# Kernel optimization log

Hardware: AMD Instinct MI355X
Metric: run time of the kernel (lower is better)

## Reference

```python
import jax, jax.numpy as jnp
import numpy as np

BETA = 0.25  # commitment_cost


def setup_inputs() -> dict:
    key = jax.random.key(0)
    k1, k2 = jax.random.split(key)
    B, T, K, D = 4096, 64, 512, 64
    z_e = jax.random.normal(k1, (B, T, D), dtype=jnp.float32)
    # torch init: uniform_(-1/K, 1/K) per slot codebook, stacked -> (T, K, D)
    codebooks = jax.random.uniform(k2, (T, K, D), dtype=jnp.float32,
                                   minval=-1.0 / K, maxval=1.0 / K)
    return {"z_e": z_e, "codebooks": codebooks}


def reference(z_e, codebooks):
    """ProductQuantizer.forward (use_ema=True, eval), vectorized over slots.

    z_e:       (B, T, D)
    codebooks: (T, K, D)
    Returns (z_q_st, tokens, vq_loss, utilization).
    """
    B, T, D = z_e.shape
    K = codebooks.shape[1]
    # squared-L2 distances per slot: (B, T, K)
    distances = (
        jnp.sum(z_e * z_e, axis=-1, keepdims=True)          # (B, T, 1)
        - 2.0 * jnp.einsum("btd,tkd->btk", z_e, codebooks)  # (B, T, K)
        + jnp.sum(codebooks * codebooks, axis=-1)[None]      # (1, T, K)
    )
    tokens = jnp.argmin(distances, axis=-1)                  # (B, T) int
    # gather nearest code per (batch, slot)
    z_q = codebooks[jnp.arange(T)[None, :], tokens]          # (B, T, D)
    # straight-through estimator
    z_q_st = z_e + jax.lax.stop_gradient(z_q - z_e)
    # use_ema=True branch: loss = mean_t( beta * mse(z_e_t, sg(z_q_t)) )
    # all slots have equal size, so this equals beta * global mean sq err
    vq_loss = BETA * jnp.mean(jnp.square(z_e - jax.lax.stop_gradient(z_q)))
    # utilization: fraction of (slot, code) pairs used at least once
    flat_idx = (jnp.arange(T)[None, :] * K + tokens).ravel()
    used = jnp.zeros((T * K,), dtype=z_e.dtype).at[flat_idx].set(1.0)
    utilization = jnp.sum(used) / (T * K)
    return z_q_st, tokens, vq_loss, utilization
```

## Files before the change

### kernel.cpp

```cpp
#include <hip/hip_runtime.h>

#define B_N 4096
#define T_N 64
#define K_N 512
#define D_N 64
#define KC 64
#define NCHUNK (K_N / KC)


__global__ __launch_bounds__(256) void prep_kernel(const float* __restrict__ cb,
                                                   float* __restrict__ c2,
                                                   unsigned* __restrict__ used,
                                                   double* __restrict__ loss) {
    int i = blockIdx.x * 256 + threadIdx.x;
    used[i] = 0u;
    if (i == 0) *loss = 0.0;
    const float4* c = reinterpret_cast<const float4*>(cb + (size_t)i * D_N);
    float s = 0.0f;
#pragma unroll
    for (int j = 0; j < 16; ++j) {
        float4 v = c[j];
        s = __fadd_rn(s, __fmul_rn(v.x, v.x));
        s = __fadd_rn(s, __fmul_rn(v.y, v.y));
        s = __fadd_rn(s, __fmul_rn(v.z, v.z));
        s = __fadd_rn(s, __fmul_rn(v.w, v.w));
    }
    c2[i] = s;
}

__global__ __launch_bounds__(256, 2) void vq_main(const float* __restrict__ z_e,
                                                  const float* __restrict__ cb,
                                                  const float* __restrict__ c2,
                                                  float* __restrict__ zq_out,
                                                  float* __restrict__ tok_out,
                                                  unsigned* __restrict__ used,
                                                  double* __restrict__ loss_sum) {
    const int t   = blockIdx.y;
    const int tid = threadIdx.x;
    const int b0  = blockIdx.x * 512 + 2 * tid;
    const int b1  = b0 + 1;

    __shared__ __align__(16) float cbuf[2][KC * D_N];
    __shared__ __align__(16) float c2buf[2][KC];

    float z0[D_N], z1[D_N];
    const float* zr0 = z_e + ((size_t)b0 * T_N + t) * D_N;
    const float* zr1 = z_e + ((size_t)b1 * T_N + t) * D_N;
#pragma unroll
    for (int j = 0; j < 16; ++j) {
        float4 v0 = reinterpret_cast<const float4*>(zr0)[j];
        float4 v1 = reinterpret_cast<const float4*>(zr1)[j];
        z0[4*j+0] = v0.x; z0[4*j+1] = v0.y; z0[4*j+2] = v0.z; z0[4*j+3] = v0.w;
        z1[4*j+0] = v1.x; z1[4*j+1] = v1.y; z1[4*j+2] = v1.z; z1[4*j+3] = v1.w;
    }

    float A0 = 0.0f, A1 = 0.0f;
#pragma unroll
    for (int d = 0; d < D_N; ++d) A0 = __fadd_rn(A0, __fmul_rn(z0[d], z0[d]));
#pragma unroll
    for (int d = 0; d < D_N; ++d) A1 = __fadd_rn(A1, __fmul_rn(z1[d], z1[d]));

    const float* cbt = cb + (size_t)t * K_N * D_N;
    const float* c2t = c2 + t * K_N;

    float4 pf[4];
    float4 c2pf;

    auto issue = [&](int c) {
        const float4* src = reinterpret_cast<const float4*>(cbt + (size_t)c * KC * D_N);
#pragma unroll
        for (int j = 0; j < 4; ++j) pf[j] = src[j * 256 + tid];
        if (tid < 16) c2pf = reinterpret_cast<const float4*>(c2t + c * KC)[tid];
    };
    auto writebuf = [&](int buf) {
#pragma unroll
        for (int j = 0; j < 4; ++j) reinterpret_cast<float4*>(cbuf[buf])[j * 256 + tid] = pf[j];
        if (tid < 16) reinterpret_cast<float4*>(c2buf[buf])[tid] = c2pf;
    };

    issue(0);
    writebuf(0);
    __syncthreads();

    float best0 = __builtin_inff(), best1 = __builtin_inff();
    int tok0 = 0, tok1 = 0;

    for (int c = 0; c < NCHUNK; ++c) {
        if (c < NCHUNK - 1) issue(c + 1);
        const float* cc  = cbuf[c & 1];
        const float* c2c = c2buf[c & 1];
        for (int kk = 0; kk < KC; ++kk) {
            const float* crow = cc + kk * D_N;
            float a0 = 0.0f, a1 = 0.0f;
#pragma unroll
            for (int d = 0; d < D_N; ++d) {
                float cd = crow[d];
                a0 = __builtin_fmaf(z0[d], cd, a0);
                a1 = __builtin_fmaf(z1[d], cd, a1);
            }
            float c2k = c2c[kk];
            float dist0 = __fadd_rn(__fsub_rn(A0, __fmul_rn(2.0f, a0)), c2k);
            float dist1 = __fadd_rn(__fsub_rn(A1, __fmul_rn(2.0f, a1)), c2k);
            int k = c * KC + kk;
            if (dist0 < best0) { best0 = dist0; tok0 = k; }
            if (dist1 < best1) { best1 = dist1; tok1 = k; }
        }
        if (c < NCHUNK - 1) {
            __syncthreads();
            writebuf((c + 1) & 1);
            __syncthreads();
        }
    }

    const float* q0 = cbt + (size_t)tok0 * D_N;
    const float* q1 = cbt + (size_t)tok1 * D_N;
    float* zq0 = zq_out + ((size_t)b0 * T_N + t) * D_N;
    float* zq1 = zq_out + ((size_t)b1 * T_N + t) * D_N;
    double ld = 0.0;
#pragma unroll
    for (int j = 0; j < 16; ++j) {
        float4 qv = reinterpret_cast<const float4*>(q0)[j];
        reinterpret_cast<float4*>(zq0)[j] = qv;
        float d0 = z0[4*j+0] - qv.x, d1 = z0[4*j+1] - qv.y;
        float d2 = z0[4*j+2] - qv.z, d3 = z0[4*j+3] - qv.w;
        ld += (double)d0*d0 + (double)d1*d1 + (double)d2*d2 + (double)d3*d3;
    }
#pragma unroll
    for (int j = 0; j < 16; ++j) {
        float4 qv = reinterpret_cast<const float4*>(q1)[j];
        reinterpret_cast<float4*>(zq1)[j] = qv;
        float d0 = z1[4*j+0] - qv.x, d1 = z1[4*j+1] - qv.y;
        float d2 = z1[4*j+2] - qv.z, d3 = z1[4*j+3] - qv.w;
        ld += (double)d0*d0 + (double)d1*d1 + (double)d2*d2 + (double)d3*d3;
    }
    tok_out[(size_t)b0 * T_N + t] = (float)tok0;
    tok_out[(size_t)b1 * T_N + t] = (float)tok1;
    used[t * K_N + tok0] = 1u;
    used[t * K_N + tok1] = 1u;

    __syncthreads();
    double* red = reinterpret_cast<double*>(cbuf[0]);
    red[tid] = ld;
    __syncthreads();
    for (int s = 128; s > 0; s >>= 1) {
        if (tid < s) red[tid] += red[tid + s];
        __syncthreads();
    }
    if (tid == 0) atomicAdd(loss_sum, red[0]);
}

__global__ __launch_bounds__(1024) void finalize_kernel(const unsigned* __restrict__ used,
                                                        const double* __restrict__ loss_sum,
                                                        float* __restrict__ out) {
    __shared__ unsigned s[1024];
    const uint4* u4 = reinterpret_cast<const uint4*>(used);
    unsigned c = 0;
#pragma unroll
    for (int i = 0; i < 8; ++i) {
        uint4 v = u4[threadIdx.x + i * 1024];
        c += v.x + v.y + v.z + v.w;
    }
    s[threadIdx.x] = c;
    __syncthreads();
    for (int st = 512; st > 0; st >>= 1) {
        if (threadIdx.x < st) s[threadIdx.x] += s[threadIdx.x + st];
        __syncthreads();
    }
    if (threadIdx.x == 0) {
        const size_t base = (size_t)B_N * T_N * D_N + (size_t)B_N * T_N;
        out[base]     = (float)(0.25 * (*loss_sum) / (double)((size_t)B_N * T_N * D_N));
        out[base + 1] = (float)s[0] / (float)(T_N * K_N);
    }
}

extern "C" void kernel_launch(void* const* d_in, const int* in_sizes, int n_in,
                              void* d_out, int out_size, void* d_ws, size_t ws_size,
                              hipStream_t stream) {
    const float* z_e = (const float*)d_in[0];
    const float* cb  = (const float*)d_in[1];
    float* out = (float*)d_out;

    float*    c2   = (float*)d_ws;
    unsigned* used = (unsigned*)((char*)d_ws + 131072);
    double*   loss = (double*)((char*)d_ws + 262144);

    prep_kernel<<<128, 256, 0, stream>>>(cb, c2, used, loss);

    float* tok_out = out + (size_t)B_N * T_N * D_N;
    vq_main<<<dim3(B_N / 512, T_N), 256, 0, stream>>>(z_e, cb, c2, out, tok_out, used, loss);

    finalize_kernel<<<1, 1024, 0, stream>>>(used, loss, out);
}
```

Before: 399.6 us.

## Read codebook rows directly from global memory and fold codebook norms into main kernel

Removes the double-buffered shared-memory staging of codebook chunks and has every thread read codebook rows straight from global memory. Each row address is uniform across the wavefront, so the loads can be served as scalar or broadcast loads through cache. Codebook squared norms are now computed per block into shared memory, which drops the separate prep kernel. The used/loss buffers are cleared with a memset instead. This trades the per-chunk block barriers for redundant norm computation in every block and a dependence on cache hits for the inner-loop loads.

```diff
diff --git a/kernel.cpp b/kernel.cpp
--- a/kernel.cpp
+++ b/kernel.cpp
@@ -4,33 +4,10 @@
 #define T_N 64
 #define K_N 512
 #define D_N 64
-#define KC 64
-#define NCHUNK (K_N / KC)
 
-
-__global__ __launch_bounds__(256) void prep_kernel(const float* __restrict__ cb,
-                                                   float* __restrict__ c2,
-                                                   unsigned* __restrict__ used,
-                                                   double* __restrict__ loss) {
-    int i = blockIdx.x * 256 + threadIdx.x;
-    used[i] = 0u;
-    if (i == 0) *loss = 0.0;
-    const float4* c = reinterpret_cast<const float4*>(cb + (size_t)i * D_N);
-    float s = 0.0f;
-#pragma unroll
-    for (int j = 0; j < 16; ++j) {
-        float4 v = c[j];
-        s = __fadd_rn(s, __fmul_rn(v.x, v.x));
-        s = __fadd_rn(s, __fmul_rn(v.y, v.y));
-        s = __fadd_rn(s, __fmul_rn(v.z, v.z));
-        s = __fadd_rn(s, __fmul_rn(v.w, v.w));
-    }
-    c2[i] = s;
-}
 
 __global__ __launch_bounds__(256, 2) void vq_main(const float* __restrict__ z_e,
                                                   const float* __restrict__ cb,
-                                                  const float* __restrict__ c2,
                                                   float* __restrict__ zq_out,
                                                   float* __restrict__ tok_out,
                                                   unsigned* __restrict__ used,
@@ -40,95 +17,92 @@
     const int b0  = blockIdx.x * 512 + 2 * tid;
     const int b1  = b0 + 1;
 
-    __shared__ __align__(16) float cbuf[2][KC * D_N];
-    __shared__ __align__(16) float c2buf[2][KC];
+    const float* cbt = cb + (size_t)t * K_N * D_N;
+
+    __shared__ float  c2s[K_N];
+    __shared__ double red[256];
+
+    {
+        const float4* c = reinterpret_cast<const float4*>(cbt) + (size_t)(2 * tid) * 16;
+        float s0 = 0.0f, s1 = 0.0f;
+#pragma unroll
+        for (int j = 0; j < 16; ++j) {
+            float4 v0 = c[j];
+            float4 v1 = c[16 + j];
+            s0 = __fadd_rn(s0, __fmul_rn(v0.x, v0.x));
+            s0 = __fadd_rn(s0, __fmul_rn(v0.y, v0.y));
+            s0 = __fadd_rn(s0, __fmul_rn(v0.z, v0.z));
+            s0 = __fadd_rn(s0, __fmul_rn(v0.w, v0.w));
+            s1 = __fadd_rn(s1, __fmul_rn(v1.x, v1.x));
+            s1 = __fadd_rn(s1, __fmul_rn(v1.y, v1.y));
+            s1 = __fadd_rn(s1, __fmul_rn(v1.z, v1.z));
+            s1 = __fadd_rn(s1, __fmul_rn(v1.w, v1.w));
+        }
+        c2s[2 * tid]     = s0;
+        c2s[2 * tid + 1] = s1;
+    }
 
     float z0[D_N], z1[D_N];
-    const float* zr0 = z_e + ((size_t)b0 * T_N + t) * D_N;
-    const float* zr1 = z_e + ((size_t)b1 * T_N + t) * D_N;
+    {
+        const float4* zr0 = reinterpret_cast<const float4*>(z_e + ((size_t)b0 * T_N + t) * D_N);
+        const float4* zr1 = reinterpret_cast<const float4*>(z_e + ((size_t)b1 * T_N + t) * D_N);
 #pragma unroll
-    for (int j = 0; j < 16; ++j) {
-        float4 v0 = reinterpret_cast<const float4*>(zr0)[j];
-        float4 v1 = reinterpret_cast<const float4*>(zr1)[j];
-        z0[4*j+0] = v0.x; z0[4*j+1] = v0.y; z0[4*j+2] = v0.z; z0[4*j+3] = v0.w;
-        z1[4*j+0] = v1.x; z1[4*j+1] = v1.y; z1[4*j+2] = v1.z; z1[4*j+3] = v1.w;
+        for (int j = 0; j < 16; ++j) {
+            float4 v0 = zr0[j];
+            float4 v1 = zr1[j];
+            z0[4*j+0] = v0.x; z0[4*j+1] = v0.y; z0[4*j+2] = v0.z; z0[4*j+3] = v0.w;
+            z1[4*j+0] = v1.x; z1[4*j+1] = v1.y; z1[4*j+2] = v1.z; z1[4*j+3] = v1.w;
+        }
+    }
+#pragma unroll
+    for (int j = 0; j < D_N; ++j) {
+        asm volatile("" : "+v"(z0[j]));
+        asm volatile("" : "+v"(z1[j]));
     }
 
     float A0 = 0.0f, A1 = 0.0f;
 #pragma unroll
-    for (int d = 0; d < D_N; ++d) A0 = __fadd_rn(A0, __fmul_rn(z0[d], z0[d]));
+    for (int j = 0; j < D_N; ++j) A0 = __fadd_rn(A0, __fmul_rn(z0[j], z0[j]));
 #pragma unroll
-    for (int d = 0; d < D_N; ++d) A1 = __fadd_rn(A1, __fmul_rn(z1[d], z1[d]));
+    for (int j = 0; j < D_N; ++j) A1 = __fadd_rn(A1, __fmul_rn(z1[j], z1[j]));
 
-    const float* cbt = cb + (size_t)t * K_N * D_N;
-    const float* c2t = c2 + t * K_N;
-
-    float4 pf[4];
-    float4 c2pf;
-
-    auto issue = [&](int c) {
-        const float4* src = reinterpret_cast<const float4*>(cbt + (size_t)c * KC * D_N);
-#pragma unroll
-        for (int j = 0; j < 4; ++j) pf[j] = src[j * 256 + tid];
-        if (tid < 16) c2pf = reinterpret_cast<const float4*>(c2t + c * KC)[tid];
-    };
-    auto writebuf = [&](int buf) {
-#pragma unroll
-        for (int j = 0; j < 4; ++j) reinterpret_cast<float4*>(cbuf[buf])[j * 256 + tid] = pf[j];
-        if (tid < 16) reinterpret_cast<float4*>(c2buf[buf])[tid] = c2pf;
-    };
-
-    issue(0);
-    writebuf(0);
     __syncthreads();
 
     float best0 = __builtin_inff(), best1 = __builtin_inff();
     int tok0 = 0, tok1 = 0;
-
-    for (int c = 0; c < NCHUNK; ++c) {
-        if (c < NCHUNK - 1) issue(c + 1);
-        const float* cc  = cbuf[c & 1];
-        const float* c2c = c2buf[c & 1];
-        for (int kk = 0; kk < KC; ++kk) {
-            const float* crow = cc + kk * D_N;
-            float a0 = 0.0f, a1 = 0.0f;
+    for (int k = 0; k < K_N; ++k) {
+        const float* crow = cbt + k * D_N;
+        float a0 = 0.0f, a1 = 0.0f;
 #pragma unroll
-            for (int d = 0; d < D_N; ++d) {
-                float cd = crow[d];
-                a0 = __builtin_fmaf(z0[d], cd, a0);
-                a1 = __builtin_fmaf(z1[d], cd, a1);
-            }
-            float c2k = c2c[kk];
-            float dist0 = __fadd_rn(__fsub_rn(A0, __fmul_rn(2.0f, a0)), c2k);
-            float dist1 = __fadd_rn(__fsub_rn(A1, __fmul_rn(2.0f, a1)), c2k);
-            int k = c * KC + kk;
-            if (dist0 < best0) { best0 = dist0; tok0 = k; }
-            if (dist1 < best1) { best1 = dist1; tok1 = k; }
+        for (int j = 0; j < D_N; ++j) {
+            float cv = crow[j];
+            a0 = __builtin_fmaf(z0[j], cv, a0);
+            a1 = __builtin_fmaf(z1[j], cv, a1);
         }
-        if (c < NCHUNK - 1) {
-            __syncthreads();
-            writebuf((c + 1) & 1);
-            __syncthreads();
-        }
+        float c2k = c2s[k];
+        float dist0 = __fadd_rn(__fsub_rn(A0, __fmul_rn(2.0f, a0)), c2k);
+        float dist1 = __fadd_rn(__fsub_rn(A1, __fmul_rn(2.0f, a1)), c2k);
+        if (dist0 < best0) { best0 = dist0; tok0 = k; }
+        if (dist1 < best1) { best1 = dist1; tok1 = k; }
     }
 
-    const float* q0 = cbt + (size_t)tok0 * D_N;
-    const float* q1 = cbt + (size_t)tok1 * D_N;
-    float* zq0 = zq_out + ((size_t)b0 * T_N + t) * D_N;
-    float* zq1 = zq_out + ((size_t)b1 * T_N + t) * D_N;
+    const float4* q0 = reinterpret_cast<const float4*>(cbt + (size_t)tok0 * D_N);
+    const float4* q1 = reinterpret_cast<const float4*>(cbt + (size_t)tok1 * D_N);
+    float4* zq0 = reinterpret_cast<float4*>(zq_out + ((size_t)b0 * T_N + t) * D_N);
+    float4* zq1 = reinterpret_cast<float4*>(zq_out + ((size_t)b1 * T_N + t) * D_N);
     double ld = 0.0;
 #pragma unroll
     for (int j = 0; j < 16; ++j) {
-        float4 qv = reinterpret_cast<const float4*>(q0)[j];
-        reinterpret_cast<float4*>(zq0)[j] = qv;
+        float4 qv = q0[j];
+        zq0[j] = qv;
         float d0 = z0[4*j+0] - qv.x, d1 = z0[4*j+1] - qv.y;
         float d2 = z0[4*j+2] - qv.z, d3 = z0[4*j+3] - qv.w;
         ld += (double)d0*d0 + (double)d1*d1 + (double)d2*d2 + (double)d3*d3;
     }
 #pragma unroll
     for (int j = 0; j < 16; ++j) {
-        float4 qv = reinterpret_cast<const float4*>(q1)[j];
-        reinterpret_cast<float4*>(zq1)[j] = qv;
+        float4 qv = q1[j];
+        zq1[j] = qv;
         float d0 = z1[4*j+0] - qv.x, d1 = z1[4*j+1] - qv.y;
         float d2 = z1[4*j+2] - qv.z, d3 = z1[4*j+3] - qv.w;
         ld += (double)d0*d0 + (double)d1*d1 + (double)d2*d2 + (double)d3*d3;
@@ -138,8 +112,6 @@
     used[t * K_N + tok0] = 1u;
     used[t * K_N + tok1] = 1u;
 
-    __syncthreads();
-    double* red = reinterpret_cast<double*>(cbuf[0]);
     red[tid] = ld;
     __syncthreads();
     for (int s = 128; s > 0; s >>= 1) {
@@ -180,14 +152,13 @@
     const float* cb  = (const float*)d_in[1];
     float* out = (float*)d_out;
 
-    float*    c2   = (float*)d_ws;
-    unsigned* used = (unsigned*)((char*)d_ws + 131072);
-    double*   loss = (double*)((char*)d_ws + 262144);
+    unsigned* used = (unsigned*)d_ws;
+    double*   loss = (double*)((char*)d_ws + 131072);
 
-    prep_kernel<<<128, 256, 0, stream>>>(cb, c2, used, loss);
+    hipMemsetAsync(used, 0, 131072 + 8, stream);
 
     float* tok_out = out + (size_t)B_N * T_N * D_N;
-    vq_main<<<dim3(B_N / 512, T_N), 256, 0, stream>>>(z_e, cb, c2, out, tok_out, used, loss);
+    vq_main<<<dim3(B_N / 512, T_N), 256, 0, stream>>>(z_e, cb, out, tok_out, used, loss);
 
     finalize_kernel<<<1, 1024, 0, stream>>>(used, loss, out);
 }
```

New measurement: 429.8 us. 1.08x slower.
